# Performance work log

Measured on AMD Instinct MI355X. Metric: run time of the kernel, lower is better.

Reference implementation:

```python
import jax, jax.numpy as jnp
import numpy as np

DIM = 768
HEADS = 12
DH = DIM // HEADS
SCALE = DH ** -0.5


def setup_inputs() -> dict:
    key = jax.random.key(0)
    ks = jax.random.split(key, 8)
    B, N = 8, 1024
    x = jax.random.normal(ks[0], (B, N, DIM), dtype=jnp.float32)
    rpb = jax.random.normal(ks[1], (1, HEADS, N, N), dtype=jnp.float32)
    s = DIM ** -0.5
    W_qkv = jax.random.normal(ks[2], (DIM, 3 * DIM), dtype=jnp.float32) * s
    W_out = jax.random.normal(ks[3], (DIM, DIM), dtype=jnp.float32) * s
    b_out = jnp.zeros((DIM,), dtype=jnp.float32)
    ln_g = jnp.ones((DIM,), dtype=jnp.float32)
    ln_b = jnp.zeros((DIM,), dtype=jnp.float32)
    return {"x": x, "relative_position_bias": rpb, "W_qkv": W_qkv,
            "W_out": W_out, "b_out": b_out, "ln_g": ln_g, "ln_b": ln_b}


def reference(x, relative_position_bias, W_qkv, W_out, b_out, ln_g, ln_b):
    # LayerNorm (eps matches torch default 1e-5)
    mu = jnp.mean(x, axis=-1, keepdims=True)
    var = jnp.mean(jnp.square(x - mu), axis=-1, keepdims=True)
    xn = (x - mu) * jax.lax.rsqrt(var + 1e-5) * ln_g + ln_b

    qkv = xn @ W_qkv                                  # [b,n,3*dim]
    q, k, v = jnp.split(qkv, 3, axis=-1)
    B, N, _ = x.shape
    reshape = lambda t: t.reshape(B, N, HEADS, DH).transpose(0, 2, 1, 3)  # b h n d
    q, k, v = reshape(q), reshape(k), reshape(v)

    scores = jnp.einsum('bhid,bhjd->bhij', q, k) * SCALE + relative_position_bias
    attn = jax.nn.softmax(scores, axis=-1)            # dropout p=0.0 -> identity
    out = jnp.einsum('bhij,bhjd->bhid', attn, v)
    out = out.transpose(0, 2, 1, 3).reshape(B, N, HEADS * DH)
    return out @ W_out + b_out
```

## Files before the change

kernel.cpp:

```cpp
#include <hip/hip_runtime.h>
#include <hip/hip_bf16.h>
#include <math.h>

#define BATCH 8
#define NSEQ  1024
#define DIMM  768
#define NHEAD 12
#define DHEAD 64
#define SCALE 0.125f
#define ROWS  (BATCH * NSEQ)

typedef __hip_bfloat16 bf16;
typedef __bf16 bf16x8 __attribute__((ext_vector_type(8)));
typedef float  f32x4  __attribute__((ext_vector_type(4)));

__global__ __launch_bounds__(256) void ln_kernel(const float* __restrict__ x,
                                                 const float* __restrict__ g,
                                                 const float* __restrict__ bta,
                                                 bf16* __restrict__ y) {
    __shared__ float ps[4], pq[4];
    __shared__ float mean_s, rstd_s;
    int row = blockIdx.x;
    int tid = threadIdx.x;
    const float* xr = x + (size_t)row * DIMM;
    float v[3];
    float s = 0.f, sq = 0.f;
#pragma unroll
    for (int i = 0; i < 3; ++i) {
        v[i] = xr[tid + 256 * i];
        s += v[i];
        sq += v[i] * v[i];
    }
#pragma unroll
    for (int off = 32; off >= 1; off >>= 1) {
        s  += __shfl_down(s, off);
        sq += __shfl_down(sq, off);
    }
    int wid = tid >> 6, lane = tid & 63;
    if (lane == 0) { ps[wid] = s; pq[wid] = sq; }
    __syncthreads();
    if (tid == 0) {
        float S = ps[0] + ps[1] + ps[2] + ps[3];
        float Q = pq[0] + pq[1] + pq[2] + pq[3];
        float mean = S * (1.0f / DIMM);
        float var  = Q * (1.0f / DIMM) - mean * mean;
        mean_s = mean;
        rstd_s = rsqrtf(fmaxf(var, 0.f) + 1e-5f);
    }
    __syncthreads();
    float mean = mean_s, rstd = rstd_s;
    bf16* yr = y + (size_t)row * DIMM;
#pragma unroll
    for (int i = 0; i < 3; ++i) {
        int c = tid + 256 * i;
        yr[c] = __float2bfloat16((v[i] - mean) * rstd * g[c] + bta[c]);
    }
}

__global__ __launch_bounds__(256) void transpose_bf16(const float* __restrict__ W,
                                                      bf16* __restrict__ Wt,
                                                      int K, int N) {
    __shared__ float t[32][33];
    int n0 = blockIdx.x * 32, k0 = blockIdx.y * 32;
    int tx = threadIdx.x, ty = threadIdx.y;
#pragma unroll
    for (int i = 0; i < 32; i += 8)
        t[ty + i][tx] = W[(size_t)(k0 + ty + i) * N + n0 + tx];
    __syncthreads();
#pragma unroll
    for (int i = 0; i < 32; i += 8)
        Wt[(size_t)(n0 + ty + i) * K + k0 + tx] = __float2bfloat16(t[tx][ty + i]);
}

template <bool OUT_BF16>
__global__ __launch_bounds__(256) void gemm_mfma(const bf16* __restrict__ A,
                                                 const bf16* __restrict__ Bt,
                                                 const float* __restrict__ bias,
                                                 void* __restrict__ Cv,
                                                 int M, int Nn, int K) {
    __shared__ bf16 As[128][40];
    __shared__ bf16 Bs[128][40];
    int tid = threadIdx.x;
    int wave = tid >> 6, lane = tid & 63, quad = lane >> 4, l16 = lane & 15;
    int wm = (wave >> 1) * 64, wn = (wave & 1) * 64;
    int m0 = blockIdx.y * 128, n0 = blockIdx.x * 128;

    f32x4 acc[4][4] = {};

    int srow = tid >> 1;
    int sk = (tid & 1) * 16;
    const bf16* Ap = A  + (size_t)(m0 + srow) * K + sk;
    const bf16* Bp = Bt + (size_t)(n0 + srow) * K + sk;

    for (int k0 = 0; k0 < K; k0 += 32) {
        uint4 a0 = *(const uint4*)(Ap + k0);
        uint4 a1 = *(const uint4*)(Ap + k0 + 8);
        uint4 b0 = *(const uint4*)(Bp + k0);
        uint4 b1 = *(const uint4*)(Bp + k0 + 8);
        __syncthreads();
        *(uint4*)&As[srow][sk]     = a0;
        *(uint4*)&As[srow][sk + 8] = a1;
        *(uint4*)&Bs[srow][sk]     = b0;
        *(uint4*)&Bs[srow][sk + 8] = b1;
        __syncthreads();
        bf16x8 af[4], bf_[4];
#pragma unroll
        for (int i = 0; i < 4; ++i) {
            af[i]  = *(const bf16x8*)&As[wm + i * 16 + l16][quad * 8];
            bf_[i] = *(const bf16x8*)&Bs[wn + i * 16 + l16][quad * 8];
        }
#pragma unroll
        for (int mi = 0; mi < 4; ++mi)
#pragma unroll
            for (int ni = 0; ni < 4; ++ni)
                acc[mi][ni] = __builtin_amdgcn_mfma_f32_16x16x32_bf16(
                    af[mi], bf_[ni], acc[mi][ni], 0, 0, 0);
    }

    float bv[4] = {0.f, 0.f, 0.f, 0.f};
    if (!OUT_BF16 && bias) {
#pragma unroll
        for (int ni = 0; ni < 4; ++ni) bv[ni] = bias[n0 + wn + ni * 16 + l16];
    }
#pragma unroll
    for (int mi = 0; mi < 4; ++mi)
#pragma unroll
        for (int reg = 0; reg < 4; ++reg) {
            size_t row = m0 + wm + mi * 16 + quad * 4 + reg;
#pragma unroll
            for (int ni = 0; ni < 4; ++ni) {
                int col = n0 + wn + ni * 16 + l16;
                float val = acc[mi][ni][reg] + bv[ni];
                if (OUT_BF16)
                    ((bf16*)Cv)[row * Nn + col] = __float2bfloat16(val);
                else
                    ((float*)Cv)[row * Nn + col] = val;
            }
        }
}

__global__ __launch_bounds__(256) void attn_mfma(const bf16* __restrict__ qkv,
                                                 const float* __restrict__ rpb,
                                                 bf16* __restrict__ outb) {
    __shared__ bf16 Ks[64][72];
    __shared__ bf16 Vt[64][72];
    __shared__ bf16 Ps[4][16][72];

    int tid = threadIdx.x;
    int wave = tid >> 6, lane = tid & 63, quad = lane >> 4, l16 = lane & 15;
    int bid = blockIdx.x;
    int mt = bid & 15;
    int bh = bid >> 4;
    int b = bh / NHEAD, h = bh % NHEAD;
    int m0 = mt * 64;

    bf16x8 qf0, qf1;
    {
        const bf16* qrow = qkv + (size_t)(b * NSEQ + m0 + wave * 16 + l16) * (3 * DIMM) + h * DHEAD;
        qf0 = *(const bf16x8*)(qrow + quad * 8);
        qf1 = *(const bf16x8*)(qrow + 32 + quad * 8);
    }
    const float* rp = rpb + ((size_t)h * NSEQ + (m0 + wave * 16)) * NSEQ;

    float m_r[4], l_r[4];
    f32x4 acco[4] = {};
#pragma unroll
    for (int r = 0; r < 4; ++r) { m_r[r] = -INFINITY; l_r[r] = 0.f; }

    int srow = tid >> 2;
    int sd = (tid & 3) * 16;

    for (int kt = 0; kt < 16; ++kt) {
        int k0 = kt * 64;
        const bf16* kbase = qkv + (size_t)(b * NSEQ + k0 + srow) * (3 * DIMM) + DIMM + h * DHEAD + sd;
        uint4 kv0 = *(const uint4*)(kbase);
        uint4 kv1 = *(const uint4*)(kbase + 8);
        uint4 vv0 = *(const uint4*)(kbase + DIMM);
        uint4 vv1 = *(const uint4*)(kbase + DIMM + 8);
        __syncthreads();
        *(uint4*)&Ks[srow][sd]     = kv0;
        *(uint4*)&Ks[srow][sd + 8] = kv1;
        union { uint4 u[2]; unsigned short us[16]; } vu;
        vu.u[0] = vv0; vu.u[1] = vv1;
#pragma unroll
        for (int j = 0; j < 16; ++j)
            *(unsigned short*)&Vt[sd + j][srow] = vu.us[j];
        __syncthreads();

        f32x4 accs[4] = {};
#pragma unroll
        for (int t = 0; t < 4; ++t) {
            bf16x8 kf0 = *(const bf16x8*)&Ks[t * 16 + l16][quad * 8];
            bf16x8 kf1 = *(const bf16x8*)&Ks[t * 16 + l16][32 + quad * 8];
            accs[t] = __builtin_amdgcn_mfma_f32_16x16x32_bf16(qf0, kf0, accs[t], 0, 0, 0);
            accs[t] = __builtin_amdgcn_mfma_f32_16x16x32_bf16(qf1, kf1, accs[t], 0, 0, 0);
        }

        float sv[4][4], mx[4];
#pragma unroll
        for (int r = 0; r < 4; ++r) mx[r] = -INFINITY;
#pragma unroll
        for (int t = 0; t < 4; ++t)
#pragma unroll
            for (int r = 0; r < 4; ++r) {
                float s = accs[t][r] * SCALE +
                          rp[(size_t)(quad * 4 + r) * NSEQ + k0 + t * 16 + l16];
                sv[t][r] = s;
                mx[r] = fmaxf(mx[r], s);
            }
#pragma unroll
        for (int off = 1; off < 16; off <<= 1)
#pragma unroll
            for (int r = 0; r < 4; ++r) mx[r] = fmaxf(mx[r], __shfl_xor(mx[r], off));
        float alpha[4], rs[4];
#pragma unroll
        for (int r = 0; r < 4; ++r) {
            float nm = fmaxf(m_r[r], mx[r]);
            alpha[r] = __expf(m_r[r] - nm);
            m_r[r] = nm;
            rs[r] = 0.f;
        }
#pragma unroll
        for (int t = 0; t < 4; ++t)
#pragma unroll
            for (int r = 0; r < 4; ++r) {
                float p = __expf(sv[t][r] - m_r[r]);
                sv[t][r] = p;
                rs[r] += p;
            }
#pragma unroll
        for (int off = 1; off < 16; off <<= 1)
#pragma unroll
            for (int r = 0; r < 4; ++r) rs[r] += __shfl_xor(rs[r], off);
#pragma unroll
        for (int r = 0; r < 4; ++r) l_r[r] = l_r[r] * alpha[r] + rs[r];
#pragma unroll
        for (int dt = 0; dt < 4; ++dt)
#pragma unroll
            for (int r = 0; r < 4; ++r) acco[dt][r] *= alpha[r];

#pragma unroll
        for (int t = 0; t < 4; ++t)
#pragma unroll
            for (int r = 0; r < 4; ++r)
                Ps[wave][quad * 4 + r][t * 16 + l16] = __float2bfloat16(sv[t][r]);
        __asm__ volatile("s_waitcnt lgkmcnt(0)" ::: "memory");

#pragma unroll
        for (int s = 0; s < 2; ++s) {
            bf16x8 pf = *(const bf16x8*)&Ps[wave][l16][s * 32 + quad * 8];
#pragma unroll
            for (int dt = 0; dt < 4; ++dt) {
                bf16x8 vf = *(const bf16x8*)&Vt[dt * 16 + l16][s * 32 + quad * 8];
                acco[dt] = __builtin_amdgcn_mfma_f32_16x16x32_bf16(pf, vf, acco[dt], 0, 0, 0);
            }
        }
    }

    float invl[4];
#pragma unroll
    for (int r = 0; r < 4; ++r) invl[r] = 1.f / l_r[r];
    bf16* orow = outb + (size_t)(b * NSEQ + m0 + wave * 16) * DIMM + h * DHEAD;
#pragma unroll
    for (int dt = 0; dt < 4; ++dt)
#pragma unroll
        for (int r = 0; r < 4; ++r)
            orow[(size_t)(quad * 4 + r) * DIMM + dt * 16 + l16] =
                __float2bfloat16(acco[dt][r] * invl[r]);
}

extern "C" void kernel_launch(void* const* d_in, const int* in_sizes, int n_in,
                              void* d_out, int out_size, void* d_ws, size_t ws_size,
                              hipStream_t stream) {
    const float* x     = (const float*)d_in[0];
    const float* rpb   = (const float*)d_in[1];
    const float* W_qkv = (const float*)d_in[2];
    const float* W_out = (const float*)d_in[3];
    const float* b_out = (const float*)d_in[4];
    const float* ln_g  = (const float*)d_in[5];
    const float* ln_b  = (const float*)d_in[6];
    float* out = (float*)d_out;

    char* p = (char*)d_ws;
    bf16* xn    = (bf16*)p; p += (size_t)ROWS * DIMM * 2;
    bf16* qkv   = (bf16*)p; p += (size_t)ROWS * 3 * DIMM * 2;
    bf16* attn  = (bf16*)p; p += (size_t)ROWS * DIMM * 2;
    bf16* WqkvT = (bf16*)p; p += (size_t)3 * DIMM * DIMM * 2;
    bf16* WoutT = (bf16*)p; p += (size_t)DIMM * DIMM * 2;

    ln_kernel<<<ROWS, 256, 0, stream>>>(x, ln_g, ln_b, xn);
    transpose_bf16<<<dim3(3 * DIMM / 32, DIMM / 32), dim3(32, 8), 0, stream>>>(
        W_qkv, WqkvT, DIMM, 3 * DIMM);
    transpose_bf16<<<dim3(DIMM / 32, DIMM / 32), dim3(32, 8), 0, stream>>>(
        W_out, WoutT, DIMM, DIMM);

    gemm_mfma<true><<<dim3(3 * DIMM / 128, ROWS / 128), 256, 0, stream>>>(
        xn, WqkvT, nullptr, qkv, ROWS, 3 * DIMM, DIMM);

    attn_mfma<<<BATCH * NHEAD * (NSEQ / 64), 256, 0, stream>>>(qkv, rpb, attn);

    gemm_mfma<false><<<dim3(DIMM / 128, ROWS / 128), 256, 0, stream>>>(
        attn, WoutT, b_out, out, ROWS, DIMM, DIMM);
}
```

Measured before the change: 299.9 us.

## Prefetch K/V tiles, compute softmax row sums via MFMA, use direct-to-LDS GEMM loads

The GEMM loads tiles with global_load_lds straight into unpadded LDS instead of staging them through registers. The attention kernel prefetches the next K/V tile into registers during compute and hoists the bias loads. It builds the V transpose with paired 32-bit LDS writes after a lane shuffle, and gets the softmax denominator from an MFMA against a ones vector instead of shuffle reductions. It also reorders the block index so blocks with the same head share the bias slice. In exchange it adds register pressure, and the unpadded GEMM LDS layout can cause bank conflicts.

```diff
diff --git a/kernel.cpp b/kernel.cpp
--- a/kernel.cpp
+++ b/kernel.cpp
@@ -13,6 +13,17 @@
 typedef __hip_bfloat16 bf16;
 typedef __bf16 bf16x8 __attribute__((ext_vector_type(8)));
 typedef float  f32x4  __attribute__((ext_vector_type(4)));
+
+#if __has_builtin(__builtin_amdgcn_global_load_lds)
+#define HAVE_GLL 1
+typedef __attribute__((address_space(3))) void lds_void_t;
+typedef const __attribute__((address_space(1))) void gbl_void_t;
+__device__ __forceinline__ void gload16(const void* g, void* l) {
+    __builtin_amdgcn_global_load_lds((gbl_void_t*)g, (lds_void_t*)l, 16, 0, 0);
+}
+#else
+#define HAVE_GLL 0
+#endif
 
 __global__ __launch_bounds__(256) void ln_kernel(const float* __restrict__ x,
                                                  const float* __restrict__ g,
@@ -78,8 +89,8 @@
                                                  const float* __restrict__ bias,
                                                  void* __restrict__ Cv,
                                                  int M, int Nn, int K) {
-    __shared__ bf16 As[128][40];
-    __shared__ bf16 Bs[128][40];
+    __shared__ bf16 As[128][32];
+    __shared__ bf16 Bs[128][32];
     int tid = threadIdx.x;
     int wave = tid >> 6, lane = tid & 63, quad = lane >> 4, l16 = lane & 15;
     int wm = (wave >> 1) * 64, wn = (wave & 1) * 64;
@@ -87,11 +98,26 @@
 
     f32x4 acc[4][4] = {};
 
+#if HAVE_GLL
+    const char* Ag = (const char*)(A  + (size_t)(m0 + (tid >> 2)) * K + (tid & 3) * 8);
+    const char* Bg = (const char*)(Bt + (size_t)(n0 + (tid >> 2)) * K + (tid & 3) * 8);
+    char* AsB = (char*)&As[0][0] + tid * 16;
+    char* BsB = (char*)&Bs[0][0] + tid * 16;
+    const size_t radv = (size_t)64 * K * 2;
+
+    for (int k0 = 0; k0 < K; k0 += 32) {
+        __syncthreads();
+        gload16(Ag, AsB);
+        gload16(Ag + radv, AsB + 4096);
+        gload16(Bg, BsB);
+        gload16(Bg + radv, BsB + 4096);
+        Ag += 64; Bg += 64;
+        __syncthreads();
+#else
     int srow = tid >> 1;
     int sk = (tid & 1) * 16;
     const bf16* Ap = A  + (size_t)(m0 + srow) * K + sk;
     const bf16* Bp = Bt + (size_t)(n0 + srow) * K + sk;
-
     for (int k0 = 0; k0 < K; k0 += 32) {
         uint4 a0 = *(const uint4*)(Ap + k0);
         uint4 a1 = *(const uint4*)(Ap + k0 + 8);
@@ -103,6 +129,7 @@
         *(uint4*)&Bs[srow][sk]     = b0;
         *(uint4*)&Bs[srow][sk + 8] = b1;
         __syncthreads();
+#endif
         bf16x8 af[4], bf_[4];
 #pragma unroll
         for (int i = 0; i < 4; ++i) {
@@ -143,15 +170,16 @@
                                                  const float* __restrict__ rpb,
                                                  bf16* __restrict__ outb) {
     __shared__ bf16 Ks[64][72];
-    __shared__ bf16 Vt[64][72];
+    __shared__ unsigned Vt32[64][36];
     __shared__ bf16 Ps[4][16][72];
 
     int tid = threadIdx.x;
     int wave = tid >> 6, lane = tid & 63, quad = lane >> 4, l16 = lane & 15;
     int bid = blockIdx.x;
-    int mt = bid & 15;
-    int bh = bid >> 4;
-    int b = bh / NHEAD, h = bh % NHEAD;
+    int b  = bid & 7;
+    int r2 = bid >> 3;
+    int h  = r2 % NHEAD;
+    int mt = r2 / NHEAD;
     int m0 = mt * 64;
 
     bf16x8 qf0, qf1;
@@ -162,30 +190,66 @@
     }
     const float* rp = rpb + ((size_t)h * NSEQ + (m0 + wave * 16)) * NSEQ;
 
-    float m_r[4], l_r[4];
+    bf16x8 onesf;
+#pragma unroll
+    for (int e = 0; e < 8; ++e) onesf[e] = (l16 == 0) ? (__bf16)1.0f : (__bf16)0.0f;
+
+    float m_r[4];
+    f32x4 accl = {0.f, 0.f, 0.f, 0.f};
     f32x4 acco[4] = {};
 #pragma unroll
-    for (int r = 0; r < 4; ++r) { m_r[r] = -INFINITY; l_r[r] = 0.f; }
+    for (int r = 0; r < 4; ++r) m_r[r] = -INFINITY;
 
     int srow = tid >> 2;
     int sd = (tid & 3) * 16;
+    bool hi = (srow & 1);
+    int p2 = srow >> 1;
+
+    const bf16* kbase = qkv + (size_t)(b * NSEQ + srow) * (3 * DIMM) + DIMM + h * DHEAD + sd;
+    uint4 kv0 = *(const uint4*)(kbase);
+    uint4 kv1 = *(const uint4*)(kbase + 8);
+    uint4 vv0 = *(const uint4*)(kbase + DIMM);
+    uint4 vv1 = *(const uint4*)(kbase + DIMM + 8);
 
     for (int kt = 0; kt < 16; ++kt) {
-        int k0 = kt * 64;
-        const bf16* kbase = qkv + (size_t)(b * NSEQ + k0 + srow) * (3 * DIMM) + DIMM + h * DHEAD + sd;
-        uint4 kv0 = *(const uint4*)(kbase);
-        uint4 kv1 = *(const uint4*)(kbase + 8);
-        uint4 vv0 = *(const uint4*)(kbase + DIMM);
-        uint4 vv1 = *(const uint4*)(kbase + DIMM + 8);
         __syncthreads();
         *(uint4*)&Ks[srow][sd]     = kv0;
         *(uint4*)&Ks[srow][sd + 8] = kv1;
-        union { uint4 u[2]; unsigned short us[16]; } vu;
-        vu.u[0] = vv0; vu.u[1] = vv1;
-#pragma unroll
-        for (int j = 0; j < 16; ++j)
-            *(unsigned short*)&Vt[sd + j][srow] = vu.us[j];
-        __syncthreads();
+        {
+            union { uint4 u4[2]; unsigned short us[16]; } vu;
+            vu.u4[0] = vv0; vu.u4[1] = vv1;
+            union { uint4 q; unsigned short h8[8]; } R, Sd;
+            Sd.q = hi ? vu.u4[0] : vu.u4[1];
+            R.q.x = __shfl_xor(Sd.q.x, 4);
+            R.q.y = __shfl_xor(Sd.q.y, 4);
+            R.q.z = __shfl_xor(Sd.q.z, 4);
+            R.q.w = __shfl_xor(Sd.q.w, 4);
+            if (!hi) {
+#pragma unroll
+                for (int j = 0; j < 8; ++j)
+                    Vt32[sd + j][p2] = (unsigned)vu.us[j] | ((unsigned)R.h8[j] << 16);
+            } else {
+#pragma unroll
+                for (int j = 0; j < 8; ++j)
+                    Vt32[sd + 8 + j][p2] = (unsigned)R.h8[j] | ((unsigned)vu.us[8 + j] << 16);
+            }
+        }
+        __syncthreads();
+
+        if (kt + 1 < 16) {
+            const bf16* kb2 = kbase + (size_t)(kt + 1) * 64 * (3 * DIMM);
+            kv0 = *(const uint4*)(kb2);
+            kv1 = *(const uint4*)(kb2 + 8);
+            vv0 = *(const uint4*)(kb2 + DIMM);
+            vv1 = *(const uint4*)(kb2 + DIMM + 8);
+        }
+        float rv[4][4];
+        const float* rpk = rp + kt * 64;
+#pragma unroll
+        for (int t = 0; t < 4; ++t)
+#pragma unroll
+            for (int r = 0; r < 4; ++r)
+                rv[t][r] = rpk[(size_t)(quad * 4 + r) * NSEQ + t * 16 + l16];
 
         f32x4 accs[4] = {};
 #pragma unroll
@@ -203,8 +267,7 @@
         for (int t = 0; t < 4; ++t)
 #pragma unroll
             for (int r = 0; r < 4; ++r) {
-                float s = accs[t][r] * SCALE +
-                          rp[(size_t)(quad * 4 + r) * NSEQ + k0 + t * 16 + l16];
+                float s = accs[t][r] * SCALE + rv[t][r];
                 sv[t][r] = s;
                 mx[r] = fmaxf(mx[r], s);
             }
@@ -212,28 +275,20 @@
         for (int off = 1; off < 16; off <<= 1)
 #pragma unroll
             for (int r = 0; r < 4; ++r) mx[r] = fmaxf(mx[r], __shfl_xor(mx[r], off));
-        float alpha[4], rs[4];
+        float alpha[4];
 #pragma unroll
         for (int r = 0; r < 4; ++r) {
             float nm = fmaxf(m_r[r], mx[r]);
             alpha[r] = __expf(m_r[r] - nm);
             m_r[r] = nm;
-            rs[r] = 0.f;
         }
 #pragma unroll
         for (int t = 0; t < 4; ++t)
 #pragma unroll
-            for (int r = 0; r < 4; ++r) {
-                float p = __expf(sv[t][r] - m_r[r]);
-                sv[t][r] = p;
-                rs[r] += p;
-            }
-#pragma unroll
-        for (int off = 1; off < 16; off <<= 1)
-#pragma unroll
-            for (int r = 0; r < 4; ++r) rs[r] += __shfl_xor(rs[r], off);
-#pragma unroll
-        for (int r = 0; r < 4; ++r) l_r[r] = l_r[r] * alpha[r] + rs[r];
+            for (int r = 0; r < 4; ++r)
+                sv[t][r] = __expf(sv[t][r] - m_r[r]);
+#pragma unroll
+        for (int r = 0; r < 4; ++r) accl[r] *= alpha[r];
 #pragma unroll
         for (int dt = 0; dt < 4; ++dt)
 #pragma unroll
@@ -246,12 +301,14 @@
                 Ps[wave][quad * 4 + r][t * 16 + l16] = __float2bfloat16(sv[t][r]);
         __asm__ volatile("s_waitcnt lgkmcnt(0)" ::: "memory");
 
+        const bf16* VtB = (const bf16*)&Vt32[0][0];
 #pragma unroll
         for (int s = 0; s < 2; ++s) {
             bf16x8 pf = *(const bf16x8*)&Ps[wave][l16][s * 32 + quad * 8];
+            accl = __builtin_amdgcn_mfma_f32_16x16x32_bf16(pf, onesf, accl, 0, 0, 0);
 #pragma unroll
             for (int dt = 0; dt < 4; ++dt) {
-                bf16x8 vf = *(const bf16x8*)&Vt[dt * 16 + l16][s * 32 + quad * 8];
+                bf16x8 vf = *(const bf16x8*)(VtB + (size_t)(dt * 16 + l16) * 72 + s * 32 + quad * 8);
                 acco[dt] = __builtin_amdgcn_mfma_f32_16x16x32_bf16(pf, vf, acco[dt], 0, 0, 0);
             }
         }
@@ -259,7 +316,10 @@
 
     float invl[4];
 #pragma unroll
-    for (int r = 0; r < 4; ++r) invl[r] = 1.f / l_r[r];
+    for (int r = 0; r < 4; ++r) {
+        float ls = __shfl(accl[r], lane & 48);
+        invl[r] = 1.f / ls;
+    }
     bf16* orow = outb + (size_t)(b * NSEQ + m0 + wave * 16) * DIMM + h * DHEAD;
 #pragma unroll
     for (int dt = 0; dt < 4; ++dt)
```

Result: faster. 290.8 us (-3.0%).
